# Kernel tuning notes

Hardware: AMD Instinct MI355X
Metric: run time of the kernel (lower is better)

## Reference

```python
import jax, jax.numpy as jnp
import numpy as np

K = 256
HEADS = 4

def setup_inputs() -> dict:
    key = jax.random.key(0)
    ks = jax.random.split(key, 6)
    x = jax.random.normal(ks[0], (4, 4096, K), dtype=jnp.float32)
    scale = 1.0 / np.sqrt(K)
    Wq = jax.random.normal(ks[1], (K, K), dtype=jnp.float32) * scale
    Wk = jax.random.normal(ks[2], (K, K), dtype=jnp.float32) * scale
    Wv = jax.random.normal(ks[3], (K, K), dtype=jnp.float32) * scale
    Wu = jax.random.normal(ks[4], (K, K), dtype=jnp.float32) * scale
    bu = jax.random.normal(ks[5], (K,), dtype=jnp.float32) * scale
    return {"x": x, "Wq": Wq, "Wk": Wk, "Wv": Wv, "Wu": Wu, "bu": bu}

def reference(x, Wq, Wk, Wv, Wu, bu):
    b, t, e = x.shape
    h = HEADS
    s = e // h
    # torch Linear: y = x @ W.T
    q = (x @ Wq.T).reshape(b, t, h, s)
    k = (x @ Wk.T).reshape(b, t, h, s)
    v = (x @ Wv.T).reshape(b, t, h, s)
    # scores: [b, h, t, t]
    dot = jnp.einsum('bihs,bjhs->bhij', q, k) / jnp.sqrt(jnp.float32(s))
    # NOTE: original code calls masked_fill (non in-place) and discards the
    # result, so the causal mask has NO effect. Faithful: no mask.
    attn = jax.nn.softmax(dot, axis=-1)
    out = jnp.einsum('bhij,bjhs->bihs', attn, v).reshape(b, t, e)
    return out @ Wu.T + bu
```

## Files before the change

kernel.cpp:

```cpp
#include <hip/hip_runtime.h>

typedef unsigned short u16;
typedef __attribute__((ext_vector_type(8))) __bf16 bf16x8;
typedef __attribute__((ext_vector_type(4))) float f32x4;
typedef __attribute__((ext_vector_type(4))) unsigned int u32x4;
typedef __attribute__((ext_vector_type(2))) unsigned int u32x2;

#define GLD16(g, l) __builtin_amdgcn_global_load_lds( \
    (const __attribute__((address_space(1))) unsigned int*)(g), \
    (__attribute__((address_space(3))) unsigned int*)(l), 16, 0, 0)

__device__ __forceinline__ u16 f2bf(float f) {
    unsigned u = __builtin_bit_cast(unsigned, f);
    unsigned r = u + 0x7fffu + ((u >> 16) & 1u);
    return (u16)(r >> 16);
}

__global__ __launch_bounds__(256) void cvt_bf16(const float* __restrict__ src,
                                                u16* __restrict__ dst, int n8) {
    int i = blockIdx.x * 256 + threadIdx.x;
    if (i >= n8) return;
    const float4* s = (const float4*)src;
    float4 a = s[2 * i], b = s[2 * i + 1];
    union { u16 u[8]; u32x4 v; } o;
    o.u[0] = f2bf(a.x); o.u[1] = f2bf(a.y); o.u[2] = f2bf(a.z); o.u[3] = f2bf(a.w);
    o.u[4] = f2bf(b.x); o.u[5] = f2bf(b.y); o.u[6] = f2bf(b.z); o.u[7] = f2bf(b.w);
    ((u32x4*)dst)[i] = o.v;
}

__global__ __launch_bounds__(256) void cvt_w4(const float* __restrict__ Wq,
                                              const float* __restrict__ Wk,
                                              const float* __restrict__ Wv,
                                              const float* __restrict__ Wu,
                                              u16* __restrict__ dst, float qscale) {
    int i = blockIdx.x * 256 + threadIdx.x;
    int widx = i >> 13, j = i & 8191;
    const float* src = (widx == 0) ? Wq : (widx == 1) ? Wk : (widx == 2) ? Wv : Wu;
    float scale = (widx == 0) ? qscale : 1.0f;
    const float4* s = (const float4*)src;
    float4 a = s[2 * j], b = s[2 * j + 1];
    union { u16 u[8]; u32x4 v; } o;
    o.u[0] = f2bf(a.x * scale); o.u[1] = f2bf(a.y * scale);
    o.u[2] = f2bf(a.z * scale); o.u[3] = f2bf(a.w * scale);
    o.u[4] = f2bf(b.x * scale); o.u[5] = f2bf(b.y * scale);
    o.u[6] = f2bf(b.z * scale); o.u[7] = f2bf(b.w * scale);
    ((u32x4*)dst)[i] = o.v;
}

template <int F32OUT>
__device__ __forceinline__ void gemm_core(const u16* __restrict__ A,
                                          const u16* __restrict__ B,
                                          void* __restrict__ Cout,
                                          const float* __restrict__ bias,
                                          size_t ldc, int mblk, int nblk,
                                          u16* As, u16* Bs) {
    const int tid = threadIdx.x;
    const int w = tid >> 6, l = tid & 63;
    const int lo = l & 15, hi = l >> 4;
    const size_t m0 = (size_t)mblk * 128;
    const int n0 = nblk * 128;
    const int wm = (w >> 1) * 64, wn = (w & 1) * 64;

    f32x4 acc[4][4] = {};

    {
#pragma unroll
        for (int i = 0; i < 2; ++i) {
            int cidx = (w * 2 + i) * 64 + l;
            int row = cidx >> 2, c = cidx & 3;
            GLD16(A + (m0 + row) * 256 + c * 8, &As[(w * 2 + i) * 512]);
            GLD16(B + (size_t)(n0 + row) * 256 + c * 8, &Bs[(w * 2 + i) * 512]);
        }
    }
    int buf = 0;
#pragma unroll 1
    for (int k0 = 0; k0 < 8; ++k0) {
        __syncthreads();
        if (k0 < 7) {
#pragma unroll
            for (int i = 0; i < 2; ++i) {
                int cidx = (w * 2 + i) * 64 + l;
                int row = cidx >> 2, c = cidx & 3;
                GLD16(A + (m0 + row) * 256 + (k0 + 1) * 32 + c * 8, &As[(buf ^ 1) * 4096 + (w * 2 + i) * 512]);
                GLD16(B + (size_t)(n0 + row) * 256 + (k0 + 1) * 32 + c * 8, &Bs[(buf ^ 1) * 4096 + (w * 2 + i) * 512]);
            }
        }
        bf16x8 af[4], bg[4];
#pragma unroll
        for (int mt = 0; mt < 4; ++mt)
            af[mt] = *(const bf16x8*)&As[buf * 4096 + (wm + mt * 16 + lo) * 32 + hi * 8];
#pragma unroll
        for (int nt = 0; nt < 4; ++nt)
            bg[nt] = *(const bf16x8*)&Bs[buf * 4096 + (wn + nt * 16 + lo) * 32 + hi * 8];
        __builtin_amdgcn_s_setprio(1);
#pragma unroll
        for (int mt = 0; mt < 4; ++mt)
#pragma unroll
            for (int nt = 0; nt < 4; ++nt)
                acc[mt][nt] = __builtin_amdgcn_mfma_f32_16x16x32_bf16(af[mt], bg[nt], acc[mt][nt], 0, 0, 0);
        __builtin_amdgcn_s_setprio(0);
        buf ^= 1;
    }

    const int r0 = hi * 4;
#pragma unroll
    for (int mt = 0; mt < 4; ++mt) {
#pragma unroll
        for (int nt = 0; nt < 4; ++nt) {
            int col = n0 + wn + nt * 16 + lo;
#pragma unroll
            for (int r = 0; r < 4; ++r) {
                size_t row = m0 + wm + mt * 16 + r0 + r;
                if (F32OUT) {
                    ((float*)Cout)[row * ldc + col] = acc[mt][nt][r] + bias[col];
                } else {
                    ((u16*)Cout)[row * ldc + col] = f2bf(acc[mt][nt][r]);
                }
            }
        }
    }
}

__global__ __launch_bounds__(256) void gemm_qkv(const u16* __restrict__ xb,
                                                const u16* __restrict__ wqb,
                                                const u16* __restrict__ wkb,
                                                const u16* __restrict__ wvb,
                                                u16* __restrict__ qb,
                                                u16* __restrict__ kb,
                                                u16* __restrict__ vtb) {
    __shared__ u16 As[2 * 4096];
    __shared__ u16 Bs[2 * 4096];
    if (blockIdx.z == 0)
        gemm_core<0>(xb, wqb, qb, nullptr, 256, blockIdx.x, blockIdx.y, As, Bs);
    else if (blockIdx.z == 1)
        gemm_core<0>(xb, wkb, kb, nullptr, 256, blockIdx.x, blockIdx.y, As, Bs);
    else
        gemm_core<0>(wvb, xb, vtb, nullptr, 16384, blockIdx.y, blockIdx.x, As, Bs);
}

__global__ __launch_bounds__(256) void wcombine(const float* __restrict__ L,
                                                float2* __restrict__ wbuf) {
    int i = blockIdx.x * 256 + threadIdx.x;
    float l0 = L[i], l1 = L[65536 + i];
    float inv = __builtin_amdgcn_rcpf(l0 + l1);
    wbuf[i] = make_float2(l0 * inv, l1 * inv);
}

template <int NS>
__global__ __launch_bounds__(256) void gemm_out(const u16* __restrict__ O0,
                                                const u16* __restrict__ O1,
                                                const float2* __restrict__ wbuf,
                                                const u16* __restrict__ Wu,
                                                float* __restrict__ out,
                                                const float* __restrict__ bias) {
    __shared__ u16 As[2][4096];
    __shared__ u16 Bs[2][4096];
    const int tid = threadIdx.x, w = tid >> 6, l = tid & 63;
    const int lo = l & 15, hi = l >> 4;
    const size_t m0 = (size_t)blockIdx.x * 128;
    const int n0 = blockIdx.y * 128;
    const int wm = (w >> 1) * 64, wn = (w & 1) * 64;
    f32x4 acc[4][4] = {};

    u32x4 aA[2], aB[2];
    float2 awt[2];
    auto loadA = [&](int k0) {
#pragma unroll
        for (int it = 0; it < 2; ++it) {
            int s = it * 256 + tid;
            int row = s >> 2, f8 = s & 3;
            size_t grow = m0 + row;
            int b = (int)(grow >> 12), q = (int)(grow & 4095);
            int feat = k0 * 32 + f8 * 8;
            int bh = b * 4 + (feat >> 6);
            size_t oidx = ((size_t)bh * 4096 + q) * 64 + (feat & 63);
            aA[it] = *(const u32x4*)(O0 + oidx);
            if (NS == 2) {
                aB[it] = *(const u32x4*)(O1 + oidx);
                awt[it] = wbuf[(size_t)bh * 4096 + q];
            }
        }
    };
    auto writeA = [&](int buf) {
#pragma unroll
        for (int it = 0; it < 2; ++it) {
            int s = it * 256 + tid;
            int row = s >> 2, f8 = s & 3;
            u32x4 v;
            if (NS == 2) {
                union { u32x4 v; __bf16 b[8]; } x, y, z;
                x.v = aA[it]; y.v = aB[it];
#pragma unroll
                for (int j = 0; j < 8; ++j)
                    z.b[j] = (__bf16)(awt[it].x * (float)x.b[j] + awt[it].y * (float)y.b[j]);
                v = z.v;
            } else {
                v = aA[it];
            }
            *(u32x4*)&As[buf][row * 32 + f8 * 8] = v;
        }
    };
    auto stageB = [&](int k0, int buf) {
#pragma unroll
        for (int i = 0; i < 2; ++i) {
            int cidx = (w * 2 + i) * 64 + l;
            int row = cidx >> 2, c = cidx & 3;
            GLD16(Wu + (size_t)(n0 + row) * 256 + k0 * 32 + c * 8, &Bs[buf][(w * 2 + i) * 512]);
        }
    };

    loadA(0); stageB(0, 0); writeA(0);
#pragma unroll 1
    for (int k0 = 0; k0 < 8; ++k0) {
        int cur = k0 & 1, nb = cur ^ 1;
        __syncthreads();
        if (k0 < 7) { stageB(k0 + 1, nb); loadA(k0 + 1); }
        bf16x8 af[4], bg[4];
#pragma unroll
        for (int mt = 0; mt < 4; ++mt)
            af[mt] = *(const bf16x8*)&As[cur][(wm + mt * 16 + lo) * 32 + hi * 8];
#pragma unroll
        for (int nt = 0; nt < 4; ++nt)
            bg[nt] = *(const bf16x8*)&Bs[cur][(wn + nt * 16 + lo) * 32 + hi * 8];
        __builtin_amdgcn_s_setprio(1);
#pragma unroll
        for (int mt = 0; mt < 4; ++mt)
#pragma unroll
            for (int nt = 0; nt < 4; ++nt)
                acc[mt][nt] = __builtin_amdgcn_mfma_f32_16x16x32_bf16(af[mt], bg[nt], acc[mt][nt], 0, 0, 0);
        __builtin_amdgcn_s_setprio(0);
        if (k0 < 7) writeA(nb);
    }

    const int r0 = hi * 4;
#pragma unroll
    for (int mt = 0; mt < 4; ++mt)
#pragma unroll
        for (int nt = 0; nt < 4; ++nt) {
            int col = n0 + wn + nt * 16 + lo;
#pragma unroll
            for (int r = 0; r < 4; ++r) {
                size_t row = m0 + wm + mt * 16 + r0 + r;
                out[row * 256 + col] = acc[mt][nt][r] + bias[col];
            }
        }
}

__global__ __launch_bounds__(256, 4) void attn_fwd(const u16* __restrict__ qb,
                                                   const u16* __restrict__ kb,
                                                   const u16* __restrict__ vtb,
                                                   u16* __restrict__ opart,
                                                   float* __restrict__ lpart,
                                                   int NT) {
    __shared__ u16 Ks[2 * 4096];
    __shared__ u16 Vs[2 * 4096];
    __shared__ u16 Ps[4 * 1024];
    const int tid = threadIdx.x, w = tid >> 6, l = tid & 63;
    const int lo = l & 15, hi = l >> 4;

    int lin = blockIdx.y * gridDim.x + blockIdx.x;
    int nid = (lin & 7) * 64 + (lin >> 3);
    const int bh = nid >> 5, qblk = nid & 31;
    const int b = bh >> 2, h = bh & 3;
    const int qbase = qblk * 128 + w * 32;
    const int kt0 = blockIdx.z * NT;
    u16* Oh = opart + (size_t)blockIdx.z * 4194304;
    float* Lh = lpart + blockIdx.z * 65536;

    bf16x8 qf[2][2];
#pragma unroll
    for (int mt = 0; mt < 2; ++mt)
#pragma unroll
        for (int ks = 0; ks < 2; ++ks)
            qf[mt][ks] = *(const bf16x8*)&qb[(size_t)(b * 4096 + qbase + mt * 16 + lo) * 256 + h * 64 + ks * 32 + hi * 8];

    float lsum[2] = {0.f, 0.f};
    f32x4 o[2][4] = {};
    const f32x4 fz = {0.f, 0.f, 0.f, 0.f};

    auto stage = [&](int sb, int kt) {
#pragma unroll
        for (int i = 0; i < 2; ++i) {
            int cidx = (w * 2 + i) * 64 + l;
            int row = cidx >> 3, c = cidx & 7;
            int sc = c ^ (row & 7);
            GLD16(kb + (size_t)(b * 4096 + kt * 64 + row) * 256 + h * 64 + sc * 8,
                  &Ks[sb * 4096 + (w * 2 + i) * 512]);
            GLD16(vtb + (size_t)(h * 64 + row) * 16384 + (size_t)b * 4096 + kt * 64 + sc * 8,
                  &Vs[sb * 4096 + (w * 2 + i) * 512]);
        }
    };

    stage(0, kt0);
    int cur = 0;
#pragma unroll 1
    for (int kt = 0; kt < NT; ++kt) {
        __syncthreads();
        if (kt + 1 < NT) stage(cur ^ 1, kt0 + kt + 1);

        f32x4 s[2][4];
        {
            bf16x8 kf[4];
#pragma unroll
            for (int nt = 0; nt < 4; ++nt) {
                int key = nt * 16 + lo;
                kf[nt] = *(const bf16x8*)&Ks[cur * 4096 + key * 64 + (hi ^ (key & 7)) * 8];
            }
            __builtin_amdgcn_s_setprio(1);
#pragma unroll
            for (int mt = 0; mt < 2; ++mt)
#pragma unroll
                for (int nt = 0; nt < 4; ++nt)
                    s[mt][nt] = __builtin_amdgcn_mfma_f32_16x16x32_bf16(kf[nt], qf[mt][0], fz, 0, 0, 0);
            __builtin_amdgcn_s_setprio(0);
        }
        {
            bf16x8 kf[4];
#pragma unroll
            for (int nt = 0; nt < 4; ++nt) {
                int key = nt * 16 + lo;
                kf[nt] = *(const bf16x8*)&Ks[cur * 4096 + key * 64 + ((4 + hi) ^ (key & 7)) * 8];
            }
            __builtin_amdgcn_s_setprio(1);
#pragma unroll
            for (int mt = 0; mt < 2; ++mt)
#pragma unroll
                for (int nt = 0; nt < 4; ++nt)
                    s[mt][nt] = __builtin_amdgcn_mfma_f32_16x16x32_bf16(kf[nt], qf[mt][1], s[mt][nt], 0, 0, 0);
            __builtin_amdgcn_s_setprio(0);
        }

        bf16x8 pf[2][2];
#pragma unroll
        for (int mt = 0; mt < 2; ++mt) {
#pragma unroll
            for (int nt = 0; nt < 4; ++nt) {
                union { __bf16 bb[4]; u32x2 v; } pw;
#pragma unroll
                for (int r = 0; r < 4; ++r) {
                    float p = __builtin_amdgcn_exp2f(s[mt][nt][r]);
                    lsum[mt] += p;
                    pw.bb[r] = (__bf16)p;
                }
                *(u32x2*)&Ps[w * 1024 + lo * 64 + (((nt * 4 + hi) ^ lo) << 2)] = pw.v;
            }
            asm volatile("s_waitcnt lgkmcnt(0)" ::: "memory");
#pragma unroll
            for (int ks2 = 0; ks2 < 2; ++ks2) {
                union { u32x2 c[2]; bf16x8 v; } pu;
                pu.c[0] = *(const u32x2*)&Ps[w * 1024 + lo * 64 + (((ks2 * 8 + hi * 2 + 0) ^ lo) << 2)];
                pu.c[1] = *(const u32x2*)&Ps[w * 1024 + lo * 64 + (((ks2 * 8 + hi * 2 + 1) ^ lo) << 2)];
                pf[mt][ks2] = pu.v;
            }
            asm volatile("s_waitcnt lgkmcnt(0)" ::: "memory");
        }

#pragma unroll
        for (int ks2 = 0; ks2 < 2; ++ks2) {
            bf16x8 vf[4];
#pragma unroll
            for (int dt = 0; dt < 4; ++dt) {
                int dr = dt * 16 + lo;
                vf[dt] = *(const bf16x8*)&Vs[cur * 4096 + dr * 64 + (((ks2 * 4 + hi) ^ (dr & 7)) << 3)];
            }
            __builtin_amdgcn_s_setprio(1);
#pragma unroll
            for (int dt = 0; dt < 4; ++dt)
                o[0][dt] = __builtin_amdgcn_mfma_f32_16x16x32_bf16(vf[dt], pf[0][ks2], o[0][dt], 0, 0, 0);
#pragma unroll
            for (int dt = 0; dt < 4; ++dt)
                o[1][dt] = __builtin_amdgcn_mfma_f32_16x16x32_bf16(vf[dt], pf[1][ks2], o[1][dt], 0, 0, 0);
            __builtin_amdgcn_s_setprio(0);
        }
        cur ^= 1;
    }

#pragma unroll
    for (int mt = 0; mt < 2; ++mt) {
        float ls = lsum[mt];
        ls += __shfl_xor(ls, 16);
        ls += __shfl_xor(ls, 32);
        float inv = __builtin_amdgcn_rcpf(ls);
        int qrow = qbase + mt * 16 + lo;
        size_t obase = ((size_t)bh * 4096 + qrow) * 64;
#pragma unroll
        for (int dt = 0; dt < 4; ++dt) {
            union { __bf16 bb[4]; u32x2 v; } ob;
#pragma unroll
            for (int r = 0; r < 4; ++r) ob.bb[r] = (__bf16)(o[mt][dt][r] * inv);
            *(u32x2*)&Oh[obase + dt * 16 + hi * 4] = ob.v;
        }
        if (hi == 0) Lh[bh * 4096 + qrow] = ls;
    }
}

extern "C" void kernel_launch(void* const* d_in, const int* in_sizes, int n_in,
                              void* d_out, int out_size, void* d_ws, size_t ws_size,
                              hipStream_t stream) {
    const float* x  = (const float*)d_in[0];
    const float* Wq = (const float*)d_in[1];
    const float* Wk = (const float*)d_in[2];
    const float* Wv = (const float*)d_in[3];
    const float* Wu = (const float*)d_in[4];
    const float* bu = (const float*)d_in[5];

    char* ws = (char*)d_ws;
    u16* xb  = (u16*)ws;
    u16* qb  = (u16*)(ws + (8u << 20));
    u16* kb  = (u16*)(ws + (16u << 20));
    u16* vtb = (u16*)(ws + (24u << 20));
    u16* wqb = (u16*)(ws + (32u << 20));
    u16* wkb = wqb + 65536;
    u16* wvb = wkb + 65536;
    u16* wub = wvb + 65536;

    const int nsplit = (ws_size >= (size_t)(50u << 20)) ? 2 : 1;
    const int NT = 64 / nsplit;
    u16* opart;
    float* lpart;
    float2* wbuf = nullptr;
    if (nsplit == 2) {
        lpart = (float*)(ws + (33u << 20));
        wbuf  = (float2*)(ws + (33u << 20) + (512u << 10));
        opart = (u16*)(ws + (34u << 20));
    } else {
        opart = xb;
        lpart = (float*)wqb;
    }

    const float kLog2eOver8 = 0.18033688011112042f;

    cvt_bf16<<<2048, 256, 0, stream>>>(x, xb, in_sizes[0] / 8);
    cvt_w4<<<128, 256, 0, stream>>>(Wq, Wk, Wv, Wu, wqb, kLog2eOver8);

    gemm_qkv<<<dim3(128, 2, 3), 256, 0, stream>>>(xb, wqb, wkb, wvb, qb, kb, vtb);

    attn_fwd<<<dim3(32, 16, nsplit), 256, 0, stream>>>(qb, kb, vtb, opart, lpart, NT);

    if (nsplit == 2) {
        wcombine<<<256, 256, 0, stream>>>(lpart, wbuf);
        gemm_out<2><<<dim3(128, 2), 256, 0, stream>>>(opart, opart + 4194304, wbuf, wub,
                                                      (float*)d_out, bu);
    } else {
        gemm_out<1><<<dim3(128, 2), 256, 0, stream>>>(opart, nullptr, nullptr, wub,
                                                      (float*)d_out, bu);
    }
}
```

Baseline: 122.1 us.

## Feed softmax probabilities directly from registers into 16x16x16 MFMA for PV

Removes the LDS round trip that reshuffled exponentiated scores into the bf16x8 operand layout. The S accumulator fragments are now reused directly as B operands of the K=16 bf16 MFMA, and the V reads are re-indexed to 4-element fragments. The row sums of P are computed with extra MFMAs against a ones vector rather than scalar adds and shuffles. The trade-off is twice as many PV MFMA instructions at half the K depth, plus two extra MFMAs per step, in exchange for dropping LDS writes, reads and waitcnt stalls. The row sum now comes from the bf16-rounded P values instead of the fp32 ones.

```diff
diff --git a/kernel.cpp b/kernel.cpp
--- a/kernel.cpp
+++ b/kernel.cpp
@@ -2,6 +2,8 @@
 
 typedef unsigned short u16;
 typedef __attribute__((ext_vector_type(8))) __bf16 bf16x8;
+typedef __attribute__((ext_vector_type(4))) __bf16 bf16x4;
+typedef __attribute__((ext_vector_type(4))) short s16x4;
 typedef __attribute__((ext_vector_type(4))) float f32x4;
 typedef __attribute__((ext_vector_type(4))) unsigned int u32x4;
 typedef __attribute__((ext_vector_type(2))) unsigned int u32x2;
@@ -254,7 +256,6 @@
                                                    int NT) {
     __shared__ u16 Ks[2 * 4096];
     __shared__ u16 Vs[2 * 4096];
-    __shared__ u16 Ps[4 * 1024];
     const int tid = threadIdx.x, w = tid >> 6, l = tid & 63;
     const int lo = l & 15, hi = l >> 4;
 
@@ -274,8 +275,9 @@
         for (int ks = 0; ks < 2; ++ks)
             qf[mt][ks] = *(const bf16x8*)&qb[(size_t)(b * 4096 + qbase + mt * 16 + lo) * 256 + h * 64 + ks * 32 + hi * 8];
 
-    float lsum[2] = {0.f, 0.f};
+    const s16x4 ones4 = {0x3F80, 0x3F80, 0x3F80, 0x3F80};
     f32x4 o[2][4] = {};
+    f32x4 osum[2] = {};
     const f32x4 fz = {0.f, 0.f, 0.f, 0.f};
 
     auto stage = [&](int sb, int kt) {
@@ -330,46 +332,36 @@
             __builtin_amdgcn_s_setprio(0);
         }
 
-        bf16x8 pf[2][2];
-#pragma unroll
-        for (int mt = 0; mt < 2; ++mt) {
+        s16x4 pf[2][4];
+#pragma unroll
+        for (int mt = 0; mt < 2; ++mt)
 #pragma unroll
             for (int nt = 0; nt < 4; ++nt) {
-                union { __bf16 bb[4]; u32x2 v; } pw;
-#pragma unroll
-                for (int r = 0; r < 4; ++r) {
-                    float p = __builtin_amdgcn_exp2f(s[mt][nt][r]);
-                    lsum[mt] += p;
-                    pw.bb[r] = (__bf16)p;
-                }
-                *(u32x2*)&Ps[w * 1024 + lo * 64 + (((nt * 4 + hi) ^ lo) << 2)] = pw.v;
-            }
-            asm volatile("s_waitcnt lgkmcnt(0)" ::: "memory");
-#pragma unroll
-            for (int ks2 = 0; ks2 < 2; ++ks2) {
-                union { u32x2 c[2]; bf16x8 v; } pu;
-                pu.c[0] = *(const u32x2*)&Ps[w * 1024 + lo * 64 + (((ks2 * 8 + hi * 2 + 0) ^ lo) << 2)];
-                pu.c[1] = *(const u32x2*)&Ps[w * 1024 + lo * 64 + (((ks2 * 8 + hi * 2 + 1) ^ lo) << 2)];
-                pf[mt][ks2] = pu.v;
-            }
-            asm volatile("s_waitcnt lgkmcnt(0)" ::: "memory");
-        }
-
-#pragma unroll
-        for (int ks2 = 0; ks2 < 2; ++ks2) {
-            bf16x8 vf[4];
+                bf16x4 t;
+#pragma unroll
+                for (int r = 0; r < 4; ++r)
+                    t[r] = (__bf16)__builtin_amdgcn_exp2f(s[mt][nt][r]);
+                pf[mt][nt] = __builtin_bit_cast(s16x4, t);
+            }
+
+#pragma unroll
+        for (int nt = 0; nt < 4; ++nt) {
+            s16x4 vf[4];
 #pragma unroll
             for (int dt = 0; dt < 4; ++dt) {
                 int dr = dt * 16 + lo;
-                vf[dt] = *(const bf16x8*)&Vs[cur * 4096 + dr * 64 + (((ks2 * 4 + hi) ^ (dr & 7)) << 3)];
+                int c8 = nt * 2 + (hi >> 1);
+                vf[dt] = *(const s16x4*)&Vs[cur * 4096 + dr * 64 + ((c8 ^ (dr & 7)) << 3) + (hi & 1) * 4];
             }
             __builtin_amdgcn_s_setprio(1);
 #pragma unroll
             for (int dt = 0; dt < 4; ++dt)
-                o[0][dt] = __builtin_amdgcn_mfma_f32_16x16x32_bf16(vf[dt], pf[0][ks2], o[0][dt], 0, 0, 0);
+                o[0][dt] = __builtin_amdgcn_mfma_f32_16x16x16bf16_1k(vf[dt], pf[0][nt], o[0][dt], 0, 0, 0);
 #pragma unroll
             for (int dt = 0; dt < 4; ++dt)
-                o[1][dt] = __builtin_amdgcn_mfma_f32_16x16x32_bf16(vf[dt], pf[1][ks2], o[1][dt], 0, 0, 0);
+                o[1][dt] = __builtin_amdgcn_mfma_f32_16x16x16bf16_1k(vf[dt], pf[1][nt], o[1][dt], 0, 0, 0);
+            osum[0] = __builtin_amdgcn_mfma_f32_16x16x16bf16_1k(ones4, pf[0][nt], osum[0], 0, 0, 0);
+            osum[1] = __builtin_amdgcn_mfma_f32_16x16x16bf16_1k(ones4, pf[1][nt], osum[1], 0, 0, 0);
             __builtin_amdgcn_s_setprio(0);
         }
         cur ^= 1;
@@ -377,9 +369,7 @@
 
 #pragma unroll
     for (int mt = 0; mt < 2; ++mt) {
-        float ls = lsum[mt];
-        ls += __shfl_xor(ls, 16);
-        ls += __shfl_xor(ls, 32);
+        float ls = osum[mt][0];
         float inv = __builtin_amdgcn_rcpf(ls);
         int qrow = qbase + mt * 16 + lo;
         size_t obase = ((size_t)bh * 4096 + qrow) * 64;
```

Result: slower. 125.2 us (+2.5%).

## Fuse conversion kernels, fold split-combine into output GEMM, compute row sums via MFMA

Applied to the files above, without the earlier changes.

The two fp32-to-bf16 conversion kernels are merged into one launch, and the separate weight-combine kernel is removed by computing the split-K softmax weights inline inside the output GEMM's A-tile load. In the attention kernel, the softmax denominator is now accumulated with an extra MFMA against a vector of ones instead of per-element scalar adds and cross-lane shuffles. This cuts two kernel launches and VALU work in the softmax inner loop. In exchange it adds two MFMAs per step and sums bf16-rounded probabilities, which is slightly different numerically from the old fp32 sums.

```diff
diff --git a/kernel.cpp b/kernel.cpp
--- a/kernel.cpp
+++ b/kernel.cpp
@@ -16,27 +16,27 @@
     return (u16)(r >> 16);
 }
 
-__global__ __launch_bounds__(256) void cvt_bf16(const float* __restrict__ src,
-                                                u16* __restrict__ dst, int n8) {
-    int i = blockIdx.x * 256 + threadIdx.x;
-    if (i >= n8) return;
-    const float4* s = (const float4*)src;
-    float4 a = s[2 * i], b = s[2 * i + 1];
-    union { u16 u[8]; u32x4 v; } o;
-    o.u[0] = f2bf(a.x); o.u[1] = f2bf(a.y); o.u[2] = f2bf(a.z); o.u[3] = f2bf(a.w);
-    o.u[4] = f2bf(b.x); o.u[5] = f2bf(b.y); o.u[6] = f2bf(b.z); o.u[7] = f2bf(b.w);
-    ((u32x4*)dst)[i] = o.v;
-}
-
-__global__ __launch_bounds__(256) void cvt_w4(const float* __restrict__ Wq,
-                                              const float* __restrict__ Wk,
-                                              const float* __restrict__ Wv,
-                                              const float* __restrict__ Wu,
-                                              u16* __restrict__ dst, float qscale) {
-    int i = blockIdx.x * 256 + threadIdx.x;
-    int widx = i >> 13, j = i & 8191;
-    const float* src = (widx == 0) ? Wq : (widx == 1) ? Wk : (widx == 2) ? Wv : Wu;
-    float scale = (widx == 0) ? qscale : 1.0f;
+__global__ __launch_bounds__(256) void cvt_all(const float* __restrict__ x,
+                                               const float* __restrict__ Wq,
+                                               const float* __restrict__ Wk,
+                                               const float* __restrict__ Wv,
+                                               const float* __restrict__ Wu,
+                                               u16* __restrict__ xb,
+                                               u16* __restrict__ wdst, float qscale) {
+    const float* src;
+    u16* dst;
+    int j;
+    float scale = 1.0f;
+    if (blockIdx.x < 2048) {
+        j = blockIdx.x * 256 + threadIdx.x;
+        src = x; dst = xb;
+    } else {
+        int i = (blockIdx.x - 2048) * 256 + threadIdx.x;
+        int widx = i >> 13; j = i & 8191;
+        src = (widx == 0) ? Wq : (widx == 1) ? Wk : (widx == 2) ? Wv : Wu;
+        if (widx == 0) scale = qscale;
+        dst = wdst + widx * 65536;
+    }
     const float4* s = (const float4*)src;
     float4 a = s[2 * j], b = s[2 * j + 1];
     union { u16 u[8]; u32x4 v; } o;
@@ -44,7 +44,7 @@
     o.u[2] = f2bf(a.z * scale); o.u[3] = f2bf(a.w * scale);
     o.u[4] = f2bf(b.x * scale); o.u[5] = f2bf(b.y * scale);
     o.u[6] = f2bf(b.z * scale); o.u[7] = f2bf(b.w * scale);
-    ((u32x4*)dst)[i] = o.v;
+    ((u32x4*)dst)[j] = o.v;
 }
 
 template <int F32OUT>
@@ -138,18 +138,10 @@
         gemm_core<0>(wvb, xb, vtb, nullptr, 16384, blockIdx.y, blockIdx.x, As, Bs);
 }
 
-__global__ __launch_bounds__(256) void wcombine(const float* __restrict__ L,
-                                                float2* __restrict__ wbuf) {
-    int i = blockIdx.x * 256 + threadIdx.x;
-    float l0 = L[i], l1 = L[65536 + i];
-    float inv = __builtin_amdgcn_rcpf(l0 + l1);
-    wbuf[i] = make_float2(l0 * inv, l1 * inv);
-}
-
 template <int NS>
 __global__ __launch_bounds__(256) void gemm_out(const u16* __restrict__ O0,
                                                 const u16* __restrict__ O1,
-                                                const float2* __restrict__ wbuf,
+                                                const float* __restrict__ lpart,
                                                 const u16* __restrict__ Wu,
                                                 float* __restrict__ out,
                                                 const float* __restrict__ bias) {
@@ -177,7 +169,10 @@
             aA[it] = *(const u32x4*)(O0 + oidx);
             if (NS == 2) {
                 aB[it] = *(const u32x4*)(O1 + oidx);
-                awt[it] = wbuf[(size_t)bh * 4096 + q];
+                float l0 = lpart[bh * 4096 + q];
+                float l1 = lpart[65536 + bh * 4096 + q];
+                float inv = __builtin_amdgcn_rcpf(l0 + l1);
+                awt[it] = make_float2(l0 * inv, l1 * inv);
             }
         }
     };
@@ -274,8 +269,12 @@
         for (int ks = 0; ks < 2; ++ks)
             qf[mt][ks] = *(const bf16x8*)&qb[(size_t)(b * 4096 + qbase + mt * 16 + lo) * 256 + h * 64 + ks * 32 + hi * 8];
 
-    float lsum[2] = {0.f, 0.f};
+    bf16x8 ones;
+#pragma unroll
+    for (int j = 0; j < 8; ++j) ones[j] = (__bf16)1.0f;
+
     f32x4 o[2][4] = {};
+    f32x4 osum[2] = {};
     const f32x4 fz = {0.f, 0.f, 0.f, 0.f};
 
     auto stage = [&](int sb, int kt) {
@@ -337,11 +336,8 @@
             for (int nt = 0; nt < 4; ++nt) {
                 union { __bf16 bb[4]; u32x2 v; } pw;
 #pragma unroll
-                for (int r = 0; r < 4; ++r) {
-                    float p = __builtin_amdgcn_exp2f(s[mt][nt][r]);
-                    lsum[mt] += p;
-                    pw.bb[r] = (__bf16)p;
-                }
+                for (int r = 0; r < 4; ++r)
+                    pw.bb[r] = (__bf16)__builtin_amdgcn_exp2f(s[mt][nt][r]);
                 *(u32x2*)&Ps[w * 1024 + lo * 64 + (((nt * 4 + hi) ^ lo) << 2)] = pw.v;
             }
             asm volatile("s_waitcnt lgkmcnt(0)" ::: "memory");
@@ -370,6 +366,8 @@
 #pragma unroll
             for (int dt = 0; dt < 4; ++dt)
                 o[1][dt] = __builtin_amdgcn_mfma_f32_16x16x32_bf16(vf[dt], pf[1][ks2], o[1][dt], 0, 0, 0);
+            osum[0] = __builtin_amdgcn_mfma_f32_16x16x32_bf16(ones, pf[0][ks2], osum[0], 0, 0, 0);
+            osum[1] = __builtin_amdgcn_mfma_f32_16x16x32_bf16(ones, pf[1][ks2], osum[1], 0, 0, 0);
             __builtin_amdgcn_s_setprio(0);
         }
         cur ^= 1;
@@ -377,9 +375,7 @@
 
 #pragma unroll
     for (int mt = 0; mt < 2; ++mt) {
-        float ls = lsum[mt];
-        ls += __shfl_xor(ls, 16);
-        ls += __shfl_xor(ls, 32);
+        float ls = osum[mt][0];
         float inv = __builtin_amdgcn_rcpf(ls);
         int qrow = qbase + mt * 16 + lo;
         size_t obase = ((size_t)bh * 4096 + qrow) * 64;
@@ -418,10 +414,8 @@
     const int NT = 64 / nsplit;
     u16* opart;
     float* lpart;
-    float2* wbuf = nullptr;
     if (nsplit == 2) {
         lpart = (float*)(ws + (33u << 20));
-        wbuf  = (float2*)(ws + (33u << 20) + (512u << 10));
         opart = (u16*)(ws + (34u << 20));
     } else {
         opart = xb;
@@ -430,16 +424,14 @@
 
     const float kLog2eOver8 = 0.18033688011112042f;
 
-    cvt_bf16<<<2048, 256, 0, stream>>>(x, xb, in_sizes[0] / 8);
-    cvt_w4<<<128, 256, 0, stream>>>(Wq, Wk, Wv, Wu, wqb, kLog2eOver8);
+    cvt_all<<<2176, 256, 0, stream>>>(x, Wq, Wk, Wv, Wu, xb, wqb, kLog2eOver8);
 
     gemm_qkv<<<dim3(128, 2, 3), 256, 0, stream>>>(xb, wqb, wkb, wvb, qb, kb, vtb);
 
     attn_fwd<<<dim3(32, 16, nsplit), 256, 0, stream>>>(qb, kb, vtb, opart, lpart, NT);
 
     if (nsplit == 2) {
-        wcombine<<<256, 256, 0, stream>>>(lpart, wbuf);
-        gemm_out<2><<<dim3(128, 2), 256, 0, stream>>>(opart, opart + 4194304, wbuf, wub,
+        gemm_out<2><<<dim3(128, 2), 256, 0, stream>>>(opart, opart + 4194304, lpart, wub,
                                                       (float*)d_out, bu);
     } else {
         gemm_out<1><<<dim3(128, 2), 256, 0, stream>>>(opart, nullptr, nullptr, wub,
```

Measured after the change: 118.5 us. 3.0% less time.
